# Kernel tuning notes

Hardware: AMD Instinct MI355X
Metric: run time of the kernel (lower is better)

The kernel has to match this reference:

```python
import jax, jax.numpy as jnp
from jax import lax
import numpy as np

B = 2; C = 128; H = 128; W = 128; NPIX = H * W
HTH = 184; HTW = 180; NBINS = HTH * HTW
NSPH = 16384; KHT = 8; KSPH = 16
N0, N1, N2 = 1024, 256, 64
K0, K1, K2 = 8, 8, 8
EPS = 1e-5


def setup_inputs() -> dict:
    key = jax.random.key(0)
    ks = jax.random.split(key, 24)
    f32 = jnp.float32
    inp = {}
    inp["image"] = jax.random.normal(ks[0], (B, C, H, W), f32)
    inp["bn_gamma"] = jnp.ones((C,), f32)
    inp["bn_beta"] = jnp.zeros((C,), f32)
    inp["ht_idx"] = jax.random.randint(ks[1], (NBINS, KHT), 0, NPIX, jnp.int32)
    inp["ht_w"] = jax.random.uniform(ks[2], (NBINS, KHT), f32)
    inp["w_htconv"] = jax.random.normal(ks[3], (3, 3, C, C), f32) / np.sqrt(9.0 * C)
    inp["htbn_gamma"] = jnp.ones((C,), f32)
    inp["htbn_beta"] = jnp.zeros((C,), f32)
    inp["sph_idx"] = jax.random.randint(ks[4], (NSPH, KSPH), 0, NBINS, jnp.int32)
    inp["sph_w"] = jax.random.uniform(ks[5], (NSPH, KSPH), f32)
    inp["w_sc"] = jax.random.normal(ks[6], (3, 64, C), f32) / np.sqrt(1.0 * C)
    inp["b_sc"] = jnp.zeros((3, 64), f32)
    inp["scbn_gamma"] = jnp.ones((3, 64), f32)
    inp["scbn_beta"] = jnp.zeros((3, 64), f32)
    inp["dgcn_w"] = jax.random.normal(ks[7], (3, 4, 128, 64), f32) / np.sqrt(128.0)
    inp["dgcn_b"] = jnp.zeros((3, 4, 64), f32)
    inp["dgcn_hw"] = jax.random.normal(ks[8], (3, 64), f32) / 8.0
    inp["dgcn_hb"] = jnp.zeros((3,), f32)
    inp["ind0"] = jax.random.randint(ks[9], (B, N0), 0, NSPH, jnp.int32)
    inp["ind1"] = jax.random.randint(ks[10], (B, 3, N1), 0, NSPH, jnp.int32)
    inp["ind2"] = jax.random.randint(ks[11], (B, 3, N2), 0, NSPH, jnp.int32)
    # kNN-style edges: structured centers (each node repeated k times), random neighbors
    c0 = jnp.tile(jnp.repeat(jnp.arange(N0, dtype=jnp.int32), K0)[None], (B, 1))
    inp["edge0"] = jnp.stack([c0, jax.random.randint(ks[12], (B, N0 * K0), 0, N0, jnp.int32)], 1)
    c1 = jnp.broadcast_to(jnp.repeat(jnp.arange(N1, dtype=jnp.int32), K1)[None, None], (B, 3, N1 * K1))
    inp["edge1"] = jnp.stack([c1, jax.random.randint(ks[13], (B, 3, N1 * K1), 0, N1, jnp.int32)], 2)
    c2 = jnp.broadcast_to(jnp.repeat(jnp.arange(N2, dtype=jnp.int32), K2)[None, None], (B, 3, N2 * K2))
    inp["edge2"] = jnp.stack([c2, jax.random.randint(ks[14], (B, 3, N2 * K2), 0, N2, jnp.int32)], 2)
    inp["target0"] = jax.random.randint(ks[15], (B, N0), 0, 2, jnp.int32)
    inp["target1"] = jax.random.randint(ks[16], (B * 3, N1), 0, 2, jnp.int32)
    inp["target2"] = jax.random.randint(ks[17], (B * 3, N2), 0, 2, jnp.int32)
    return inp


def _bn2d(x, g, b):
    m = x.mean((0, 2, 3), keepdims=True)
    v = x.var((0, 2, 3), keepdims=True)
    return g[None, :, None, None] * (x - m) * lax.rsqrt(v + EPS) + b[None, :, None, None]


def _sphere(x_htf, sph_idx, sph_w, ind):
    # x_htf: [B,C,NBINS]; ind: [B,S] -> weighted gather of HT bins per sphere node
    mi = sph_idx[ind]          # [B,S,K]
    mw = sph_w[ind]            # [B,S,K]
    g = jax.vmap(lambda xb, ib: xb[:, ib])(x_htf, mi)   # [B,C,S,K]
    return (g * mw[:, None]).sum(-1)                    # [B,C,S]


def _sconv(x, w, b, g, be):
    # 1x1 conv [B,C,S]->[B,64,S] + BN1d (batch stats) + ReLU
    y = jnp.einsum('oc,bcs->bos', w, x) + b[None, :, None]
    m = y.mean((0, 2), keepdims=True)
    v = y.var((0, 2), keepdims=True)
    return jax.nn.relu(g[None, :, None] * (y - m) * lax.rsqrt(v + EPS) + be[None, :, None])


def _dgcn(x, edge, ws, bs, hw, hb, n, k):
    # x: [Bg,n,64]; edge: [Bg,2,n*k] (row0=center, row1=neighbor); 4 EdgeConv layers
    for i in range(4):
        xc = jnp.take_along_axis(x, edge[:, 0, :, None], axis=1)   # [Bg,n*k,Cin]
        xn = jnp.take_along_axis(x, edge[:, 1, :, None], axis=1)
        h = jax.nn.relu(jnp.concatenate([xc, xn - xc], -1) @ ws[i] + bs[i])
        x = h.reshape(x.shape[0], n, k, -1).max(2)                 # max over neighbors
    return x @ hw + hb                                             # [Bg,n] logits


def _bce(logits, target):
    t = target.astype(logits.dtype)
    l = jnp.maximum(logits, 0.0) - logits * t + jnp.log1p(jnp.exp(-jnp.abs(logits)))
    pos = t > 0.5
    npos = jnp.maximum(pos.sum(), 1).astype(l.dtype)
    nneg = jnp.maximum((~pos).sum(), 1).astype(l.dtype)
    return jnp.where(pos, l, 0.0).sum() / npos, jnp.where(pos, 0.0, l).sum() / nneg


def _forward(image, bn_gamma, bn_beta, ht_idx, ht_w, w_htconv, htbn_gamma, htbn_beta,
             sph_idx, sph_w, w_sc, b_sc, scbn_gamma, scbn_beta,
             dgcn_w, dgcn_b, dgcn_hw, dgcn_hb,
             ind0, ind1, ind2, edge0, edge1, edge2, target0, target1, target2):
    x = jax.nn.relu(_bn2d(image, bn_gamma, bn_beta))
    xf = x.reshape(B, C, NPIX)
    # Hough voting: each HT bin accumulates KHT weighted pixels
    ht = (xf[:, :, ht_idx] * ht_w).sum(-1).reshape(B, C, HTH, HTW)
    hc = lax.conv_general_dilated(ht, w_htconv, (1, 1), 'SAME',
                                  dimension_numbers=('NCHW', 'HWIO', 'NCHW'))
    x_htf = jax.nn.relu(_bn2d(hc, htbn_gamma, htbn_beta)).reshape(B, C, NBINS)

    # scale 0
    x0 = _sconv(_sphere(x_htf, sph_idx, sph_w, ind0),
                w_sc[0], b_sc[0], scbn_gamma[0], scbn_beta[0]).transpose(0, 2, 1)
    x0 = _dgcn(x0, edge0, dgcn_w[0], dgcn_b[0], dgcn_hw[0], dgcn_hb[0], N0, K0)   # [B,N0]
    # scale 1 (3 vanishing-point branches folded into batch)
    x1 = _sconv(_sphere(x_htf, sph_idx, sph_w, ind1.reshape(B, -1)),
                w_sc[1], b_sc[1], scbn_gamma[1], scbn_beta[1]).transpose(0, 2, 1)
    x1 = _dgcn(x1.reshape(B * 3, N1, 64), edge1.reshape(B * 3, 2, N1 * K1),
               dgcn_w[1], dgcn_b[1], dgcn_hw[1], dgcn_hb[1], N1, K1)              # [B*3,N1]
    # scale 2
    x2 = _sconv(_sphere(x_htf, sph_idx, sph_w, ind2.reshape(B, -1)),
                w_sc[2], b_sc[2], scbn_gamma[2], scbn_beta[2]).transpose(0, 2, 1)
    x2 = _dgcn(x2.reshape(B * 3, N2, 64), edge2.reshape(B * 3, 2, N2 * K2),
               dgcn_w[2], dgcn_b[2], dgcn_hw[2], dgcn_hb[2], N2, K2)              # [B*3,N2]

    lp0, ln0 = _bce(x0, target0)
    lp1, ln1 = _bce(x1, target1)
    lp2, ln2 = _bce(x2, target2)
    losses = jnp.stack([lp0, ln0, lp1, ln1, lp2, ln2])
    preds = jnp.concatenate([jax.nn.sigmoid(x0).reshape(B, -1),
                             jax.nn.sigmoid(x1).reshape(B, -1),
                             jax.nn.sigmoid(x2).reshape(B, -1)], axis=1)
    return losses, preds


def reference(image, bn_gamma, bn_beta, ht_idx, ht_w, w_htconv, htbn_gamma, htbn_beta,
              sph_idx, sph_w, w_sc, b_sc, scbn_gamma, scbn_beta,
              dgcn_w, dgcn_b, dgcn_hw, dgcn_hb,
              ind0, ind1, ind2, edge0, edge1, edge2, target0, target1, target2):
    return _forward(image, bn_gamma, bn_beta, ht_idx, ht_w, w_htconv, htbn_gamma, htbn_beta,
                    sph_idx, sph_w, w_sc, b_sc, scbn_gamma, scbn_beta,
                    dgcn_w, dgcn_b, dgcn_hw, dgcn_hb,
                    ind0, ind1, ind2, edge0, edge1, edge2, target0, target1, target2)
```

## Files before the change

kernel.cpp:

```cpp
#include <hip/hip_runtime.h>
#include <math.h>

#define B_ 2
#define C_ 128
#define NPIX_ 16384
#define HTH_ 184
#define HTW_ 180
#define NBINS_ 33120
#define PH_ 186
#define PW_ 184
#define NPB_ 1984
#define TOTN_ 3968
#define EPS_ 1e-5f

#define ST_HC_SUM 0
#define ST_HC_SQ  128
#define ST_SC_SUM 256
#define ST_SC_SQ  448
#define ST_LOSS   640
#define ST_IMG_S1 1472
#define ST_IMG_S2 1600

typedef __attribute__((ext_vector_type(8))) short v8s;
typedef __attribute__((ext_vector_type(4))) float v4f;

__device__ inline unsigned short f2b(float f) {
  unsigned u = __builtin_bit_cast(unsigned, f);
  unsigned r = u + 0x7fffu + ((u >> 16) & 1u);
  return (unsigned short)(r >> 16);
}
__device__ inline float b2f(unsigned short u) {
  unsigned v = ((unsigned)u) << 16;
  return __builtin_bit_cast(float, v);
}

__global__ void kprep(const float* __restrict__ w, const float* __restrict__ dw,
                      unsigned short* __restrict__ wtb, unsigned short* __restrict__ dwb,
                      unsigned* __restrict__ htb2) {
  int idx = blockIdx.x*256 + threadIdx.x;
  if (idx < 147456) {
    int tap = idx >> 14, z = idx & 16383;
    int j = z & 7, lane = (z >> 3) & 63, nt = (z >> 9) & 7, kt = (z >> 12) & 3;
    int l = lane & 15, q = lane >> 4;
    int co = nt*16 + l, ci = kt*32 + q*8 + j;
    wtb[idx] = f2b(w[(tap*C_ + ci)*C_ + co]);
  } else if (idx < 245760) {
    int i2 = idx - 147456;
    int sl = i2 >> 13, z = i2 & 8191;
    int j = z & 7, lane = (z >> 3) & 63, nt = (z >> 9) & 3, kt = (z >> 11) & 3;
    int l = lane & 15, q = lane >> 4;
    int co = nt*16 + l, cc = kt*32 + q*8 + j;
    dwb[i2] = f2b(dw[(sl*128 + cc)*64 + co]);
  } else {
    int i = idx - 245760;
    int d = i & 63;
    int cell = i >> 6;
    int b = cell / 1112, j = cell % 1112;
    int y, x;
    if (j < 184) { y = 0; x = j; }
    else if (j < 368) { y = 185; x = j - 184; }
    else { int c = j - 368; int xi = c / 186; y = c % 186; x = xi == 0 ? 0 : 180 + xi; }
    htb2[((size_t)(b*PH_ + y)*PW_ + x)*64 + d] = 0u;
  }
}

__global__ void k1_img_stats(const float* __restrict__ img, float* __restrict__ st) {
  int c = blockIdx.x; int chunk = blockIdx.y; int tid = threadIdx.x;
  float s1 = 0.f, s2 = 0.f;
  for (int i = chunk*4096 + tid; i < (chunk+1)*4096; i += 256) {
    int b = i >> 14, p = i & (NPIX_-1);
    float v = img[((size_t)(b*C_ + c))*NPIX_ + p];
    s1 += v; s2 += v*v;
  }
  __shared__ float r1[256], r2[256];
  r1[tid] = s1; r2[tid] = s2; __syncthreads();
  for (int off = 128; off; off >>= 1) {
    if (tid < off) { r1[tid] += r1[tid+off]; r2[tid] += r2[tid+off]; }
    __syncthreads();
  }
  if (tid == 0) {
    atomicAdd(&st[ST_IMG_S1 + c], r1[0]);
    atomicAdd(&st[ST_IMG_S2 + c], r2[0]);
  }
}

__global__ void k2_bnrelu_t(const float* __restrict__ img, const float* __restrict__ st,
                            const float* __restrict__ g, const float* __restrict__ be,
                            unsigned short* __restrict__ xt) {
  __shared__ float tile[32*65];
  __shared__ float ash[32], dsh[32];
  int p0 = blockIdx.x*64, c0 = blockIdx.y*32, b = blockIdx.z;
  int tid = threadIdx.x;
  if (tid < 32) {
    int c = c0 + tid;
    float n = (float)(B_*NPIX_);
    float m = st[ST_IMG_S1+c]/n;
    float var = st[ST_IMG_S2+c]/n - m*m;
    float a = g[c]*rsqrtf(var + EPS_);
    ash[tid] = a; dsh[tid] = be[c] - a*m;
  }
  __syncthreads();
  for (int r = 0; r < 8; r++) {
    int flat = tid + r*256;
    int row = flat >> 6, col = flat & 63;
    float v = img[((size_t)(b*C_ + c0 + row))*NPIX_ + p0 + col];
    tile[row*65 + col] = fmaxf(ash[row]*v + dsh[row], 0.f);
  }
  __syncthreads();
  for (int r = 0; r < 4; r++) {
    int flat = (tid + r*256)*2;
    int pl = flat >> 5, cl = flat & 31;
    unsigned lo = f2b(tile[cl*65 + pl]);
    unsigned hi = f2b(tile[(cl+1)*65 + pl]);
    *(unsigned*)&xt[((size_t)b*NPIX_ + p0 + pl)*C_ + c0 + cl] = lo | (hi << 16);
  }
}

__global__ void k3_hough(const unsigned* __restrict__ xt2, const int* __restrict__ hidx,
                         const float* __restrict__ hwt, unsigned* __restrict__ htb2) {
  int tid = threadIdx.x;
  int wv = __builtin_amdgcn_readfirstlane(tid >> 6);
  int bin = blockIdx.x*4 + wv;
  int b = blockIdx.y;
  int lane = tid & 63;
  const unsigned* base = xt2 + (size_t)b*NPIX_*64 + lane;
  float acc0 = 0.f, acc1 = 0.f;
  #pragma unroll
  for (int k = 0; k < 8; k++) {
    int p = hidx[bin*8 + k];
    float w = hwt[bin*8 + k];
    unsigned dv = base[(size_t)p*64];
    acc0 += w * b2f((unsigned short)(dv & 0xffff));
    acc1 += w * b2f((unsigned short)(dv >> 16));
  }
  int y = bin / HTW_, x = bin - y*HTW_;
  unsigned lo = f2b(acc0), hi = f2b(acc1);
  htb2[((size_t)(b*PH_ + y + 1)*PW_ + (x+1))*64 + lane] = lo | (hi << 16);
}

__global__ __launch_bounds__(256, 4) void k4_mfma(
    const unsigned short* __restrict__ htb, const unsigned short* __restrict__ wtb,
    unsigned short* __restrict__ hcb, float* __restrict__ st) {
  __shared__ char smem[33792];
  int tid = threadIdx.x;
  int w = tid >> 6, lane = tid & 63;
  int quad = lane >> 4, l16 = lane & 15;
  int ph = w & 1, ch = w >> 1;
  int b = blockIdx.z;
  int x0 = blockIdx.x*64;
  int y0 = blockIdx.y*2;
  const v8s* wbase = (const v8s*)wtb + lane;
  v4f acc[4][4];
  #pragma unroll
  for (int t = 0; t < 4; t++)
    #pragma unroll
    for (int nt = 0; nt < 4; nt++) acc[t][nt] = (v4f){0,0,0,0};

  for (int half = 0; half < 2; half++) {
    __syncthreads();
    #pragma unroll
    for (int it = 0; it < 9; it++) {
      int c = tid + it*256;
      if (c < 2112) {
        int px = c >> 3, part = c & 7;
        int r = px/66, xc = px - r*66;
        int gx = x0 + xc; if (gx > PW_-1) gx = PW_-1;
        const uint4* gp = (const uint4*)(htb + (((size_t)(b*PH_ + y0 + r))*PW_ + gx)*C_ + half*64) + part;
        *(uint4*)(smem + px*128 + ((part ^ (xc & 7)) << 4)) = *gp;
      }
    }
    __syncthreads();
    #pragma unroll
    for (int dy = 0; dy < 3; dy++) {
      #pragma unroll
      for (int dx = 0; dx < 3; dx++) {
        int sw = ((l16 + dx) & 7) << 4;
        int rowbase = ((ph + dy)*66 + l16 + dx)*128;
        #pragma unroll
        for (int kt2 = 0; kt2 < 2; kt2++) {
          int qo = quad*16 + kt2*64;
          v8s a[4];
          #pragma unroll
          for (int t = 0; t < 4; t++)
            a[t] = *(const v8s*)(smem + rowbase + t*2048 + (qo ^ sw));
          int kt = half*2 + kt2;
          #pragma unroll
          for (int nt = 0; nt < 4; nt++) {
            v8s bf = wbase[(((dy*3 + dx)*4 + kt)*8 + ch*4 + nt)*64];
            #pragma unroll
            for (int t = 0; t < 4; t++)
              acc[t][nt] = __builtin_amdgcn_mfma_f32_16x16x32_bf16(a[t], bf, acc[t][nt], 0, 0, 0);
          }
        }
      }
    }
  }
  __syncthreads();
  float* red = (float*)smem;
  int y = y0 + ph;
  float s1[4] = {0,0,0,0}, s2[4] = {0,0,0,0};
  #pragma unroll
  for (int t = 0; t < 4; t++) {
    #pragma unroll
    for (int nt = 0; nt < 4; nt++) {
      int co = ch*64 + nt*16 + l16;
      #pragma unroll
      for (int reg = 0; reg < 4; reg++) {
        int x = x0 + t*16 + quad*4 + reg;
        if (x < HTW_) {
          float v = acc[t][nt][reg];
          hcb[((size_t)b*NBINS_ + y*HTW_ + x)*C_ + co] = f2b(v);
          s1[nt] += v; s2[nt] += v*v;
        }
      }
    }
  }
  int slot = ph*4 + quad;
  #pragma unroll
  for (int nt = 0; nt < 4; nt++) red[(ch*64 + nt*16 + l16)*9 + slot] = s1[nt];
  __syncthreads();
  if (tid < 128) {
    float s = 0.f;
    #pragma unroll
    for (int k = 0; k < 8; k++) s += red[tid*9 + k];
    atomicAdd(&st[ST_HC_SUM + tid], s);
  }
  __syncthreads();
  #pragma unroll
  for (int nt = 0; nt < 4; nt++) red[(ch*64 + nt*16 + l16)*9 + slot] = s2[nt];
  __syncthreads();
  if (tid < 128) {
    float s = 0.f;
    #pragma unroll
    for (int k = 0; k < 8; k++) s += red[tid*9 + k];
    atomicAdd(&st[ST_HC_SQ + tid], s);
  }
}

__global__ void k6_sphere(const unsigned* __restrict__ hcb2, const float* __restrict__ st,
                          const float* __restrict__ g, const float* __restrict__ be,
                          const int* __restrict__ sph_idx, const float* __restrict__ sph_w,
                          const int* __restrict__ ind0, const int* __restrict__ ind1,
                          const int* __restrict__ ind2, float* __restrict__ out) {
  int tid = threadIdx.x;
  int wv = __builtin_amdgcn_readfirstlane(tid >> 6);
  int gn = blockIdx.x*4 + wv;
  int lane = tid & 63;
  int b = gn / NPB_, nb = gn % NPB_;
  int v;
  if (nb < 1024) v = ind0[b*1024 + nb];
  else if (nb < 1792) v = ind1[b*768 + nb - 1024];
  else v = ind2[b*192 + nb - 1792];
  int c0 = lane*2, c1 = c0 + 1;
  float n = (float)(B_*NBINS_);
  float m0 = st[ST_HC_SUM + c0]/n, m1 = st[ST_HC_SUM + c1]/n;
  float va0 = st[ST_HC_SQ + c0]/n - m0*m0, va1 = st[ST_HC_SQ + c1]/n - m1*m1;
  float a0 = g[c0]*rsqrtf(va0 + EPS_), a1 = g[c1]*rsqrtf(va1 + EPS_);
  float d0 = be[c0] - a0*m0, d1 = be[c1] - a1*m1;
  const unsigned* base = hcb2 + (size_t)b*NBINS_*64 + lane;
  float acc0 = 0.f, acc1 = 0.f;
  #pragma unroll
  for (int k = 0; k < 16; k++) {
    int mi = sph_idx[v*16 + k];
    float mw = sph_w[v*16 + k];
    unsigned dv = base[(size_t)mi*64];
    acc0 += mw * fmaxf(a0*b2f((unsigned short)(dv & 0xffff)) + d0, 0.f);
    acc1 += mw * fmaxf(a1*b2f((unsigned short)(dv >> 16)) + d1, 0.f);
  }
  *(float2*)&out[(size_t)gn*C_ + c0] = make_float2(acc0, acc1);
}

__global__ __launch_bounds__(256) void k7_sconv(
    const float* __restrict__ xin, const float* __restrict__ w_sc,
    const float* __restrict__ b_sc, float* __restrict__ y, float* __restrict__ st) {
  __shared__ float xs[32*128];
  __shared__ float wT[128*65];
  __shared__ float red[256];
  int tid = threadIdx.x;
  int gn0 = blockIdx.x * 32;
  int nb = gn0 % NPB_;
  int s = nb < 1024 ? 0 : (nb < 1792 ? 1 : 2);
  for (int r = 0; r < 16; r++) {
    int flat = tid + r*256;
    xs[flat] = xin[(size_t)gn0*C_ + flat];
  }
  for (int r = 0; r < 32; r++) {
    int flat = tid + r*256;
    int o = flat >> 7, cc = flat & 127;
    wT[cc*65 + o] = w_sc[(s*64 + o)*C_ + cc];
  }
  __syncthreads();
  int o = tid & 63, nl = tid >> 6;
  float bias = b_sc[s*64 + o];
  float acc[8];
  #pragma unroll
  for (int i = 0; i < 8; i++) acc[i] = bias;
  for (int cc = 0; cc < 128; cc++) {
    float wv = wT[cc*65 + o];
    #pragma unroll
    for (int i = 0; i < 8; i++)
      acc[i] += xs[(nl*8 + i)*128 + cc] * wv;
  }
  float s1 = 0.f, s2 = 0.f;
  #pragma unroll
  for (int i = 0; i < 8; i++) {
    y[(size_t)(gn0 + nl*8 + i)*64 + o] = acc[i];
    s1 += acc[i]; s2 += acc[i]*acc[i];
  }
  red[tid] = s1; __syncthreads();
  if (nl == 0) atomicAdd(&st[ST_SC_SUM + s*64 + o], red[o] + red[64+o] + red[128+o] + red[192+o]);
  __syncthreads();
  red[tid] = s2; __syncthreads();
  if (nl == 0) atomicAdd(&st[ST_SC_SQ + s*64 + o], red[o] + red[64+o] + red[128+o] + red[192+o]);
}

__global__ __launch_bounds__(256) void k10_dgcn(
    const void* __restrict__ xin_, unsigned short* __restrict__ xout,
    const int* __restrict__ edge0, const int* __restrict__ edge1, const int* __restrict__ edge2,
    const unsigned short* __restrict__ dwb, const float* __restrict__ db,
    const float* __restrict__ st, const float* __restrict__ scg, const float* __restrict__ scb,
    int layer, int usebn) {
  __shared__ unsigned short E[128*136];
  __shared__ float ash[64], dsh[64];
  int tid = threadIdx.x;
  int bid = blockIdx.x;
  int s, node_base, le_blk, span; const int* ec;
  if (bid < 128) {
    s = 0; int b = bid >> 6; node_base = b*NPB_; le_blk = (bid & 63)*128;
    span = 8192; ec = edge0 + b*2*8192;
  } else if (bid < 224) {
    int j = bid - 128; s = 1; int seg = j >> 4; int b = seg/3, vp = seg%3;
    node_base = b*NPB_ + 1024 + vp*256; le_blk = (j & 15)*128;
    span = 2048; ec = edge1 + ((b*3+vp)*2)*2048;
  } else {
    int j = bid - 224; s = 2; int seg = j >> 2; int b = seg/3, vp = seg%3;
    node_base = b*NPB_ + 1792 + vp*64; le_blk = (j & 3)*128;
    span = 512; ec = edge2 + ((b*3+vp)*2)*512;
  }
  const int* en = ec + span;
  if (usebn) {
    if (tid < 64) {
      float n = s==0 ? 2048.f : (s==1 ? 1536.f : 384.f);
      float m = st[ST_SC_SUM + s*64 + tid]/n;
      float var = st[ST_SC_SQ + s*64 + tid]/n - m*m;
      float a = scg[s*64 + tid]*rsqrtf(var + EPS_);
      ash[tid] = a; dsh[tid] = scb[s*64 + tid] - a*m;
    }
    __syncthreads();
  }
  {
    int r = tid >> 1, h = tid & 1;
    int e = le_blk + r;
    int ci = ec[e], ni = en[e];
    if (usebn) {
      const float* xc = (const float*)xin_ + (size_t)(node_base + ci)*64;
      const float* xn = (const float*)xin_ + (size_t)(node_base + ni)*64;
      #pragma unroll
      for (int c8 = 0; c8 < 64; c8 += 8) {
        v8s pk;
        #pragma unroll
        for (int j = 0; j < 8; j++) {
          int c = c8 + j;
          float vc = fmaxf(ash[c]*xc[c] + dsh[c], 0.f);
          float val = vc;
          if (h) val = fmaxf(ash[c]*xn[c] + dsh[c], 0.f) - vc;
          pk[j] = (short)f2b(val);
        }
        *(v8s*)&E[r*136 + h*64 + c8] = pk;
      }
    } else {
      const unsigned short* xc = (const unsigned short*)xin_ + (size_t)(node_base + ci)*64;
      const unsigned short* xn = (const unsigned short*)xin_ + (size_t)(node_base + ni)*64;
      #pragma unroll
      for (int c8 = 0; c8 < 64; c8 += 8) {
        v8s vc8 = *(const v8s*)&xc[c8];
        v8s pk = vc8;
        if (h) {
          v8s vn8 = *(const v8s*)&xn[c8];
          #pragma unroll
          for (int j = 0; j < 8; j++)
            pk[j] = (short)f2b(b2f((unsigned short)vn8[j]) - b2f((unsigned short)vc8[j]));
        }
        *(v8s*)&E[r*136 + h*64 + c8] = pk;
      }
    }
  }
  __syncthreads();
  int wave = tid >> 6, lane = tid & 63;
  int quad = lane >> 4, l16 = lane & 15;
  const unsigned short* wb = dwb + (size_t)(s*4 + layer)*8192;
  v4f acc[2][4];
  #pragma unroll
  for (int t = 0; t < 2; t++)
    #pragma unroll
    for (int nt = 0; nt < 4; nt++) acc[t][nt] = (v4f){0,0,0,0};
  #pragma unroll
  for (int kt = 0; kt < 4; kt++) {
    v8s a0 = *(const v8s*)&E[(wave*32 + l16)*136 + quad*8 + kt*32];
    v8s a1 = *(const v8s*)&E[(wave*32 + 16 + l16)*136 + quad*8 + kt*32];
    #pragma unroll
    for (int nt = 0; nt < 4; nt++) {
      v8s bf = *(const v8s*)&wb[((kt*4 + nt)*64 + lane)*8];
      acc[0][nt] = __builtin_amdgcn_mfma_f32_16x16x32_bf16(a0, bf, acc[0][nt], 0, 0, 0);
      acc[1][nt] = __builtin_amdgcn_mfma_f32_16x16x32_bf16(a1, bf, acc[1][nt], 0, 0, 0);
    }
  }
  int vb0 = le_blk/8 + wave*4;
  #pragma unroll
  for (int t = 0; t < 2; t++) {
    #pragma unroll
    for (int nt = 0; nt < 4; nt++) {
      float bias = db[(s*4 + layer)*64 + nt*16 + l16];
      float m = fmaxf(fmaxf(acc[t][nt][0], acc[t][nt][1]),
                      fmaxf(acc[t][nt][2], acc[t][nt][3]));
      m = fmaxf(m + bias, 0.f);
      float other = __shfl_xor(m, 16);
      m = fmaxf(m, other);
      if ((quad & 1) == 0) {
        int v = vb0 + t*2 + (quad >> 1);
        xout[(size_t)(node_base + v)*64 + nt*16 + l16] = f2b(m);
      }
    }
  }
}

__global__ __launch_bounds__(256) void k11_head(
    const unsigned short* __restrict__ x, const float* __restrict__ hw, const float* __restrict__ hb,
    const int* __restrict__ t0, const int* __restrict__ t1, const int* __restrict__ t2,
    float* __restrict__ out, float* __restrict__ st) {
  __shared__ float shw[192];
  int tid = threadIdx.x;
  if (tid < 192) shw[tid] = hw[tid];
  __syncthreads();
  int gn = blockIdx.x*256 + tid;
  bool valid = gn < TOTN_;
  int g = valid ? gn : TOTN_-1;
  int b = g / NPB_, nb = g % NPB_;
  int s, tg;
  if (nb < 1024) { s = 0; tg = t0[b*1024 + nb]; }
  else if (nb < 1792) { s = 1; int j = nb-1024; tg = t1[(b*3 + (j>>8))*256 + (j&255)]; }
  else { s = 2; int j = nb-1792; tg = t2[(b*3 + (j>>6))*64 + (j&63)]; }
  const unsigned short* row = x + (size_t)g*64;
  float logit = hb[s];
  #pragma unroll
  for (int c8 = 0; c8 < 64; c8 += 8) {
    v8s v = *(const v8s*)&row[c8];
    #pragma unroll
    for (int j = 0; j < 8; j++)
      logit += b2f((unsigned short)v[j]) * shw[s*64 + c8 + j];
  }
  if (valid) out[6 + gn] = 1.f / (1.f + expf(-logit));
  float tf = (float)tg;
  float l = fmaxf(logit, 0.f) - logit*tf + log1pf(expf(-fabsf(logit)));
  float sp = (valid && tg) ? l : 0.f;
  float sn = (valid && !tg) ? l : 0.f;
  float cp = (valid && tg) ? 1.f : 0.f;
  float cn = (valid && !tg) ? 1.f : 0.f;
  for (int off = 32; off; off >>= 1) {
    sp += __shfl_down(sp, off);
    sn += __shfl_down(sn, off);
    cp += __shfl_down(cp, off);
    cn += __shfl_down(cn, off);
  }
  if ((tid & 63) == 0) {
    atomicAdd(&st[ST_LOSS + s*4 + 0], sp);
    atomicAdd(&st[ST_LOSS + s*4 + 1], sn);
    atomicAdd(&st[ST_LOSS + s*4 + 2], cp);
    atomicAdd(&st[ST_LOSS + s*4 + 3], cn);
  }
}

__global__ void k12_fin(const float* __restrict__ st, float* __restrict__ out) {
  int i = threadIdx.x;
  if (i < 6) {
    int s = i >> 1; int pos = !(i & 1);
    float sum = st[ST_LOSS + s*4 + (pos ? 0 : 1)];
    float cnt = st[ST_LOSS + s*4 + (pos ? 2 : 3)];
    out[i] = sum / fmaxf(cnt, 1.f);
  }
}

extern "C" void kernel_launch(void* const* d_in, const int* in_sizes, int n_in,
                              void* d_out, int out_size, void* d_ws, size_t ws_size,
                              hipStream_t stream) {
  const float* image  = (const float*)d_in[0];
  const float* bn_g   = (const float*)d_in[1];
  const float* bn_b   = (const float*)d_in[2];
  const int*   ht_idx = (const int*)  d_in[3];
  const float* ht_w   = (const float*)d_in[4];
  const float* w_conv = (const float*)d_in[5];
  const float* htbn_g = (const float*)d_in[6];
  const float* htbn_b = (const float*)d_in[7];
  const int*   sph_idx= (const int*)  d_in[8];
  const float* sph_w  = (const float*)d_in[9];
  const float* w_sc   = (const float*)d_in[10];
  const float* b_sc   = (const float*)d_in[11];
  const float* scbn_g = (const float*)d_in[12];
  const float* scbn_b = (const float*)d_in[13];
  const float* dgcn_w = (const float*)d_in[14];
  const float* dgcn_b = (const float*)d_in[15];
  const float* dgcn_hw= (const float*)d_in[16];
  const float* dgcn_hb= (const float*)d_in[17];
  const int*   ind0   = (const int*)  d_in[18];
  const int*   ind1   = (const int*)  d_in[19];
  const int*   ind2   = (const int*)  d_in[20];
  const int*   edge0  = (const int*)  d_in[21];
  const int*   edge1  = (const int*)  d_in[22];
  const int*   edge2  = (const int*)  d_in[23];
  const int*   t0     = (const int*)  d_in[24];
  const int*   t1     = (const int*)  d_in[25];
  const int*   t2     = (const int*)  d_in[26];
  float* out = (float*)d_out;

  char* ws = (char*)d_ws;
  unsigned short* x_t   = (unsigned short*)(ws);
  unsigned short* htb   = (unsigned short*)(ws +  8388608);
  unsigned short* hcb   = (unsigned short*)(ws + 25911296);
  unsigned short* wtb   = (unsigned short*)(ws + 42868736);
  unsigned short* dwb   = (unsigned short*)(ws + 43163648);
  float*          sph_o = (float*)(ws + 43360256);
  float*          y_sc  = (float*)(ws + 45391872);
  unsigned short* xdgA  = (unsigned short*)(ws + 46407680);
  unsigned short* xdgB  = (unsigned short*)(ws + 46915584);
  float*          st    = (float*)(ws + 47423488);

  hipMemsetAsync(st, 0, 1728*sizeof(float), stream);
  kprep<<<1516, 256, 0, stream>>>(w_conv, dgcn_w, wtb, dwb, (unsigned*)htb);
  k1_img_stats<<<dim3(128,8), 256, 0, stream>>>(image, st);
  k2_bnrelu_t<<<dim3(256,4,2), 256, 0, stream>>>(image, st, bn_g, bn_b, x_t);
  k3_hough<<<dim3(NBINS_/4, B_), 256, 0, stream>>>((const unsigned*)x_t, ht_idx, ht_w, (unsigned*)htb);
  k4_mfma<<<dim3(3, 92, 2), 256, 0, stream>>>(htb, wtb, hcb, st);
  k6_sphere<<<TOTN_/4, 256, 0, stream>>>((const unsigned*)hcb, st, htbn_g, htbn_b, sph_idx, sph_w, ind0, ind1, ind2, sph_o);
  k7_sconv<<<TOTN_/32, 256, 0, stream>>>(sph_o, w_sc, b_sc, y_sc, st);
  k10_dgcn<<<248, 256, 0, stream>>>((const void*)y_sc, xdgA, edge0, edge1, edge2, dwb, dgcn_b, st, scbn_g, scbn_b, 0, 1);
  k10_dgcn<<<248, 256, 0, stream>>>((const void*)xdgA, xdgB, edge0, edge1, edge2, dwb, dgcn_b, st, scbn_g, scbn_b, 1, 0);
  k10_dgcn<<<248, 256, 0, stream>>>((const void*)xdgB, xdgA, edge0, edge1, edge2, dwb, dgcn_b, st, scbn_g, scbn_b, 2, 0);
  k10_dgcn<<<248, 256, 0, stream>>>((const void*)xdgA, xdgB, edge0, edge1, edge2, dwb, dgcn_b, st, scbn_g, scbn_b, 3, 0);
  k11_head<<<16, 256, 0, stream>>>(xdgB, dgcn_hw, dgcn_hb, t0, t1, t2, out, st);
  k12_fin<<<1, 64, 0, stream>>>(st, out);
}
```

Before: 267.8 us.

## Fuse prep with image stats, restructure conv MFMA, fuse sphere gather with sconv

Merges the weight/padding prep kernel with the image-statistics kernel into one launch. Rewrites the 3x3 Hough conv so each wave computes 32 flat output bins across all 128 output channels, loading activations straight from global memory and staging only each tap's weights in shared memory. Fuses the sphere gather with the sphere conv so gathered features stay in shared memory instead of round-tripping through a global buffer. This trades the earlier shared-memory halo reuse of activations for simpler indexing and fewer launches, and the fused sphere kernel now has far fewer blocks to spread the gather work over.

Result: faster. 249.3 us (-6.9%).

```diff
diff --git a/kernel.cpp b/kernel.cpp
--- a/kernel.cpp
+++ b/kernel.cpp
@@ -34,53 +34,57 @@
   return __builtin_bit_cast(float, v);
 }
 
-__global__ void kprep(const float* __restrict__ w, const float* __restrict__ dw,
-                      unsigned short* __restrict__ wtb, unsigned short* __restrict__ dwb,
-                      unsigned* __restrict__ htb2) {
-  int idx = blockIdx.x*256 + threadIdx.x;
-  if (idx < 147456) {
-    int tap = idx >> 14, z = idx & 16383;
-    int j = z & 7, lane = (z >> 3) & 63, nt = (z >> 9) & 7, kt = (z >> 12) & 3;
-    int l = lane & 15, q = lane >> 4;
-    int co = nt*16 + l, ci = kt*32 + q*8 + j;
-    wtb[idx] = f2b(w[(tap*C_ + ci)*C_ + co]);
-  } else if (idx < 245760) {
-    int i2 = idx - 147456;
-    int sl = i2 >> 13, z = i2 & 8191;
-    int j = z & 7, lane = (z >> 3) & 63, nt = (z >> 9) & 3, kt = (z >> 11) & 3;
-    int l = lane & 15, q = lane >> 4;
-    int co = nt*16 + l, cc = kt*32 + q*8 + j;
-    dwb[i2] = f2b(dw[(sl*128 + cc)*64 + co]);
+__global__ void kprep0(const float* __restrict__ w, const float* __restrict__ dw,
+                       unsigned short* __restrict__ wtb, unsigned short* __restrict__ dwb,
+                       unsigned* __restrict__ htb2, const float* __restrict__ img,
+                       float* __restrict__ st) {
+  int bid = blockIdx.x;
+  int tid = threadIdx.x;
+  if (bid < 1516) {
+    int idx = bid*256 + tid;
+    if (idx < 147456) {
+      int tap = idx >> 14, z = idx & 16383;
+      int j = z & 7, lane = (z >> 3) & 63, nt = (z >> 9) & 7, kt = (z >> 12) & 3;
+      int l = lane & 15, q = lane >> 4;
+      int co = nt*16 + l, ci = kt*32 + q*8 + j;
+      wtb[idx] = f2b(w[(tap*C_ + ci)*C_ + co]);
+    } else if (idx < 245760) {
+      int i2 = idx - 147456;
+      int sl = i2 >> 13, z = i2 & 8191;
+      int j = z & 7, lane = (z >> 3) & 63, nt = (z >> 9) & 3, kt = (z >> 11) & 3;
+      int l = lane & 15, q = lane >> 4;
+      int co = nt*16 + l, cc = kt*32 + q*8 + j;
+      dwb[i2] = f2b(dw[(sl*128 + cc)*64 + co]);
+    } else if (idx < 388096) {
+      int i = idx - 245760;
+      int d = i & 63;
+      int cell = i >> 6;
+      int b = cell / 1112, j = cell % 1112;
+      int y, x;
+      if (j < 184) { y = 0; x = j; }
+      else if (j < 368) { y = 185; x = j - 184; }
+      else { int c = j - 368; int xi = c / 186; y = c % 186; x = xi == 0 ? 0 : 180 + xi; }
+      htb2[((size_t)(b*PH_ + y)*PW_ + x)*64 + d] = 0u;
+    }
   } else {
-    int i = idx - 245760;
-    int d = i & 63;
-    int cell = i >> 6;
-    int b = cell / 1112, j = cell % 1112;
-    int y, x;
-    if (j < 184) { y = 0; x = j; }
-    else if (j < 368) { y = 185; x = j - 184; }
-    else { int c = j - 368; int xi = c / 186; y = c % 186; x = xi == 0 ? 0 : 180 + xi; }
-    htb2[((size_t)(b*PH_ + y)*PW_ + x)*64 + d] = 0u;
-  }
-}
-
-__global__ void k1_img_stats(const float* __restrict__ img, float* __restrict__ st) {
-  int c = blockIdx.x; int chunk = blockIdx.y; int tid = threadIdx.x;
-  float s1 = 0.f, s2 = 0.f;
-  for (int i = chunk*4096 + tid; i < (chunk+1)*4096; i += 256) {
-    int b = i >> 14, p = i & (NPIX_-1);
-    float v = img[((size_t)(b*C_ + c))*NPIX_ + p];
-    s1 += v; s2 += v*v;
-  }
-  __shared__ float r1[256], r2[256];
-  r1[tid] = s1; r2[tid] = s2; __syncthreads();
-  for (int off = 128; off; off >>= 1) {
-    if (tid < off) { r1[tid] += r1[tid+off]; r2[tid] += r2[tid+off]; }
-    __syncthreads();
-  }
-  if (tid == 0) {
-    atomicAdd(&st[ST_IMG_S1 + c], r1[0]);
-    atomicAdd(&st[ST_IMG_S2 + c], r2[0]);
+    int kb = bid - 1516;
+    int c = kb >> 3, chunk = kb & 7;
+    float s1 = 0.f, s2 = 0.f;
+    for (int i = chunk*4096 + tid; i < (chunk+1)*4096; i += 256) {
+      int b = i >> 14, p = i & (NPIX_-1);
+      float v = img[((size_t)(b*C_ + c))*NPIX_ + p];
+      s1 += v; s2 += v*v;
+    }
+    __shared__ float r1[256], r2[256];
+    r1[tid] = s1; r2[tid] = s2; __syncthreads();
+    for (int off = 128; off; off >>= 1) {
+      if (tid < off) { r1[tid] += r1[tid+off]; r2[tid] += r2[tid+off]; }
+      __syncthreads();
+    }
+    if (tid == 0) {
+      atomicAdd(&st[ST_IMG_S1 + c], r1[0]);
+      atomicAdd(&st[ST_IMG_S2 + c], r2[0]);
+    }
   }
 }
 
@@ -138,151 +142,139 @@
   htb2[((size_t)(b*PH_ + y + 1)*PW_ + (x+1))*64 + lane] = lo | (hi << 16);
 }
 
-__global__ __launch_bounds__(256, 4) void k4_mfma(
+__global__ __launch_bounds__(256, 3) void k4_mfma(
     const unsigned short* __restrict__ htb, const unsigned short* __restrict__ wtb,
     unsigned short* __restrict__ hcb, float* __restrict__ st) {
-  __shared__ char smem[33792];
-  int tid = threadIdx.x;
-  int w = tid >> 6, lane = tid & 63;
+  __shared__ char smem[32768];
+  int tid = threadIdx.x;
+  int wav = tid >> 6, lane = tid & 63;
   int quad = lane >> 4, l16 = lane & 15;
-  int ph = w & 1, ch = w >> 1;
-  int b = blockIdx.z;
-  int x0 = blockIdx.x*64;
-  int y0 = blockIdx.y*2;
-  const v8s* wbase = (const v8s*)wtb + lane;
-  v4f acc[4][4];
-  #pragma unroll
-  for (int t = 0; t < 4; t++)
-    #pragma unroll
-    for (int nt = 0; nt < 4; nt++) acc[t][nt] = (v4f){0,0,0,0};
-
-  for (int half = 0; half < 2; half++) {
+  int b = blockIdx.y;
+  int p0 = blockIdx.x*128 + wav*32;
+  size_t ab[2];
+  #pragma unroll
+  for (int t = 0; t < 2; t++) {
+    int px = p0 + t*16 + l16; if (px > NBINS_-1) px = NBINS_-1;
+    int y = px / HTW_, x = px % HTW_;
+    ab[t] = (((size_t)(b*PH_ + y))*PW_ + x)*C_ + quad*8;
+  }
+  v4f acc[2][8];
+  #pragma unroll
+  for (int t = 0; t < 2; t++)
+    #pragma unroll
+    for (int nt = 0; nt < 8; nt++) acc[t][nt] = (v4f){0,0,0,0};
+
+  for (int tap = 0; tap < 9; tap++) {
     __syncthreads();
-    #pragma unroll
-    for (int it = 0; it < 9; it++) {
-      int c = tid + it*256;
-      if (c < 2112) {
-        int px = c >> 3, part = c & 7;
-        int r = px/66, xc = px - r*66;
-        int gx = x0 + xc; if (gx > PW_-1) gx = PW_-1;
-        const uint4* gp = (const uint4*)(htb + (((size_t)(b*PH_ + y0 + r))*PW_ + gx)*C_ + half*64) + part;
-        *(uint4*)(smem + px*128 + ((part ^ (xc & 7)) << 4)) = *gp;
+    const uint4* src = (const uint4*)(wtb + tap*16384);
+    uint4* dst = (uint4*)smem;
+    #pragma unroll
+    for (int s = 0; s < 8; s++) dst[tid + s*256] = src[tid + s*256];
+    __syncthreads();
+    int dy = tap/3, dx = tap - dy*3;
+    int toff = (dy*PW_ + dx)*C_;
+    v8s a[2][4];
+    #pragma unroll
+    for (int t = 0; t < 2; t++)
+      #pragma unroll
+      for (int kt = 0; kt < 4; kt++)
+        a[t][kt] = *(const v8s*)&htb[ab[t] + toff + kt*32];
+    #pragma unroll
+    for (int kt = 0; kt < 4; kt++) {
+      #pragma unroll
+      for (int nt = 0; nt < 8; nt++) {
+        v8s bf = *(const v8s*)(smem + ((((kt*8 + nt)*64) + lane) << 4));
+        acc[0][nt] = __builtin_amdgcn_mfma_f32_16x16x32_bf16(a[0][kt], bf, acc[0][nt], 0, 0, 0);
+        acc[1][nt] = __builtin_amdgcn_mfma_f32_16x16x32_bf16(a[1][kt], bf, acc[1][nt], 0, 0, 0);
       }
     }
-    __syncthreads();
-    #pragma unroll
-    for (int dy = 0; dy < 3; dy++) {
-      #pragma unroll
-      for (int dx = 0; dx < 3; dx++) {
-        int sw = ((l16 + dx) & 7) << 4;
-        int rowbase = ((ph + dy)*66 + l16 + dx)*128;
-        #pragma unroll
-        for (int kt2 = 0; kt2 < 2; kt2++) {
-          int qo = quad*16 + kt2*64;
-          v8s a[4];
-          #pragma unroll
-          for (int t = 0; t < 4; t++)
-            a[t] = *(const v8s*)(smem + rowbase + t*2048 + (qo ^ sw));
-          int kt = half*2 + kt2;
-          #pragma unroll
-          for (int nt = 0; nt < 4; nt++) {
-            v8s bf = wbase[(((dy*3 + dx)*4 + kt)*8 + ch*4 + nt)*64];
-            #pragma unroll
-            for (int t = 0; t < 4; t++)
-              acc[t][nt] = __builtin_amdgcn_mfma_f32_16x16x32_bf16(a[t], bf, acc[t][nt], 0, 0, 0);
-          }
-        }
-      }
-    }
   }
   __syncthreads();
   float* red = (float*)smem;
-  int y = y0 + ph;
-  float s1[4] = {0,0,0,0}, s2[4] = {0,0,0,0};
-  #pragma unroll
-  for (int t = 0; t < 4; t++) {
-    #pragma unroll
-    for (int nt = 0; nt < 4; nt++) {
-      int co = ch*64 + nt*16 + l16;
+  float s1[8], s2[8];
+  #pragma unroll
+  for (int nt = 0; nt < 8; nt++) { s1[nt] = 0.f; s2[nt] = 0.f; }
+  #pragma unroll
+  for (int t = 0; t < 2; t++) {
+    int pbase = p0 + t*16 + quad*4;
+    #pragma unroll
+    for (int nt = 0; nt < 8; nt++) {
+      int co = nt*16 + l16;
       #pragma unroll
       for (int reg = 0; reg < 4; reg++) {
-        int x = x0 + t*16 + quad*4 + reg;
-        if (x < HTW_) {
+        int po = pbase + reg;
+        if (po < NBINS_) {
           float v = acc[t][nt][reg];
-          hcb[((size_t)b*NBINS_ + y*HTW_ + x)*C_ + co] = f2b(v);
+          hcb[((size_t)b*NBINS_ + po)*C_ + co] = f2b(v);
           s1[nt] += v; s2[nt] += v*v;
         }
       }
     }
   }
-  int slot = ph*4 + quad;
-  #pragma unroll
-  for (int nt = 0; nt < 4; nt++) red[(ch*64 + nt*16 + l16)*9 + slot] = s1[nt];
+  int slot = wav*4 + quad;
+  #pragma unroll
+  for (int nt = 0; nt < 8; nt++) red[(nt*16 + l16)*17 + slot] = s1[nt];
   __syncthreads();
   if (tid < 128) {
     float s = 0.f;
     #pragma unroll
-    for (int k = 0; k < 8; k++) s += red[tid*9 + k];
+    for (int k = 0; k < 16; k++) s += red[tid*17 + k];
     atomicAdd(&st[ST_HC_SUM + tid], s);
   }
   __syncthreads();
   #pragma unroll
-  for (int nt = 0; nt < 4; nt++) red[(ch*64 + nt*16 + l16)*9 + slot] = s2[nt];
+  for (int nt = 0; nt < 8; nt++) red[(nt*16 + l16)*17 + slot] = s2[nt];
   __syncthreads();
   if (tid < 128) {
     float s = 0.f;
     #pragma unroll
-    for (int k = 0; k < 8; k++) s += red[tid*9 + k];
+    for (int k = 0; k < 16; k++) s += red[tid*17 + k];
     atomicAdd(&st[ST_HC_SQ + tid], s);
   }
 }
 
-__global__ void k6_sphere(const unsigned* __restrict__ hcb2, const float* __restrict__ st,
-                          const float* __restrict__ g, const float* __restrict__ be,
-                          const int* __restrict__ sph_idx, const float* __restrict__ sph_w,
-                          const int* __restrict__ ind0, const int* __restrict__ ind1,
-                          const int* __restrict__ ind2, float* __restrict__ out) {
-  int tid = threadIdx.x;
-  int wv = __builtin_amdgcn_readfirstlane(tid >> 6);
-  int gn = blockIdx.x*4 + wv;
-  int lane = tid & 63;
-  int b = gn / NPB_, nb = gn % NPB_;
-  int v;
-  if (nb < 1024) v = ind0[b*1024 + nb];
-  else if (nb < 1792) v = ind1[b*768 + nb - 1024];
-  else v = ind2[b*192 + nb - 1792];
-  int c0 = lane*2, c1 = c0 + 1;
-  float n = (float)(B_*NBINS_);
-  float m0 = st[ST_HC_SUM + c0]/n, m1 = st[ST_HC_SUM + c1]/n;
-  float va0 = st[ST_HC_SQ + c0]/n - m0*m0, va1 = st[ST_HC_SQ + c1]/n - m1*m1;
-  float a0 = g[c0]*rsqrtf(va0 + EPS_), a1 = g[c1]*rsqrtf(va1 + EPS_);
-  float d0 = be[c0] - a0*m0, d1 = be[c1] - a1*m1;
-  const unsigned* base = hcb2 + (size_t)b*NBINS_*64 + lane;
-  float acc0 = 0.f, acc1 = 0.f;
-  #pragma unroll
-  for (int k = 0; k < 16; k++) {
-    int mi = sph_idx[v*16 + k];
-    float mw = sph_w[v*16 + k];
-    unsigned dv = base[(size_t)mi*64];
-    acc0 += mw * fmaxf(a0*b2f((unsigned short)(dv & 0xffff)) + d0, 0.f);
-    acc1 += mw * fmaxf(a1*b2f((unsigned short)(dv >> 16)) + d1, 0.f);
-  }
-  *(float2*)&out[(size_t)gn*C_ + c0] = make_float2(acc0, acc1);
-}
-
-__global__ __launch_bounds__(256) void k7_sconv(
-    const float* __restrict__ xin, const float* __restrict__ w_sc,
-    const float* __restrict__ b_sc, float* __restrict__ y, float* __restrict__ st) {
+__global__ __launch_bounds__(256) void k67_sphconv(
+    const unsigned* __restrict__ hcb2, const float* __restrict__ g, const float* __restrict__ be,
+    const int* __restrict__ sph_idx, const float* __restrict__ sph_w,
+    const int* __restrict__ ind0, const int* __restrict__ ind1, const int* __restrict__ ind2,
+    const float* __restrict__ w_sc, const float* __restrict__ b_sc,
+    float* __restrict__ y, float* __restrict__ st) {
   __shared__ float xs[32*128];
   __shared__ float wT[128*65];
   __shared__ float red[256];
   int tid = threadIdx.x;
-  int gn0 = blockIdx.x * 32;
-  int nb = gn0 % NPB_;
-  int s = nb < 1024 ? 0 : (nb < 1792 ? 1 : 2);
-  for (int r = 0; r < 16; r++) {
-    int flat = tid + r*256;
-    xs[flat] = xin[(size_t)gn0*C_ + flat];
+  int gn0 = blockIdx.x*32;
+  int nb0 = gn0 % NPB_;
+  int s = nb0 < 1024 ? 0 : (nb0 < 1792 ? 1 : 2);
+  int wv = tid >> 6, lane = tid & 63;
+  {
+    int c0 = lane*2, c1 = c0 + 1;
+    float n = (float)(B_*NBINS_);
+    float m0 = st[ST_HC_SUM + c0]/n, m1 = st[ST_HC_SUM + c1]/n;
+    float va0 = st[ST_HC_SQ + c0]/n - m0*m0, va1 = st[ST_HC_SQ + c1]/n - m1*m1;
+    float a0 = g[c0]*rsqrtf(va0 + EPS_), a1 = g[c1]*rsqrtf(va1 + EPS_);
+    float d0 = be[c0] - a0*m0, d1 = be[c1] - a1*m1;
+    for (int i = 0; i < 8; i++) {
+      int node_l = wv*8 + i;
+      int gn = gn0 + node_l;
+      int b = gn / NPB_, nb = gn % NPB_;
+      int v;
+      if (nb < 1024) v = ind0[b*1024 + nb];
+      else if (nb < 1792) v = ind1[b*768 + nb - 1024];
+      else v = ind2[b*192 + nb - 1792];
+      v = __builtin_amdgcn_readfirstlane(v);
+      const unsigned* base = hcb2 + (size_t)b*NBINS_*64 + lane;
+      float acc0 = 0.f, acc1 = 0.f;
+      #pragma unroll
+      for (int k = 0; k < 16; k++) {
+        int mi = sph_idx[v*16 + k];
+        float mw = sph_w[v*16 + k];
+        unsigned dv = base[(size_t)mi*64];
+        acc0 += mw * fmaxf(a0*b2f((unsigned short)(dv & 0xffff)) + d0, 0.f);
+        acc1 += mw * fmaxf(a1*b2f((unsigned short)(dv >> 16)) + d1, 0.f);
+      }
+      *(float2*)&xs[node_l*128 + c0] = make_float2(acc0, acc1);
+    }
   }
   for (int r = 0; r < 32; r++) {
     int flat = tid + r*256;
@@ -296,10 +288,10 @@
   #pragma unroll
   for (int i = 0; i < 8; i++) acc[i] = bias;
   for (int cc = 0; cc < 128; cc++) {
-    float wv = wT[cc*65 + o];
+    float wvv = wT[cc*65 + o];
     #pragma unroll
     for (int i = 0; i < 8; i++)
-      acc[i] += xs[(nl*8 + i)*128 + cc] * wv;
+      acc[i] += xs[(nl*8 + i)*128 + cc] * wvv;
   }
   float s1 = 0.f, s2 = 0.f;
   #pragma unroll
@@ -518,20 +510,18 @@
   unsigned short* hcb   = (unsigned short*)(ws + 25911296);
   unsigned short* wtb   = (unsigned short*)(ws + 42868736);
   unsigned short* dwb   = (unsigned short*)(ws + 43163648);
-  float*          sph_o = (float*)(ws + 43360256);
-  float*          y_sc  = (float*)(ws + 45391872);
-  unsigned short* xdgA  = (unsigned short*)(ws + 46407680);
-  unsigned short* xdgB  = (unsigned short*)(ws + 46915584);
-  float*          st    = (float*)(ws + 47423488);
+  float*          y_sc  = (float*)(ws + 43360256);
+  unsigned short* xdgA  = (unsigned short*)(ws + 44376064);
+  unsigned short* xdgB  = (unsigned short*)(ws + 44883968);
+  float*          st    = (float*)(ws + 45391872);
 
   hipMemsetAsync(st, 0, 1728*sizeof(float), stream);
-  kprep<<<1516, 256, 0, stream>>>(w_conv, dgcn_w, wtb, dwb, (unsigned*)htb);
-  k1_img_stats<<<dim3(128,8), 256, 0, stream>>>(image, st);
+  kprep0<<<2540, 256, 0, stream>>>(w_conv, dgcn_w, wtb, dwb, (unsigned*)htb, image, st);
   k2_bnrelu_t<<<dim3(256,4,2), 256, 0, stream>>>(image, st, bn_g, bn_b, x_t);
   k3_hough<<<dim3(NBINS_/4, B_), 256, 0, stream>>>((const unsigned*)x_t, ht_idx, ht_w, (unsigned*)htb);
-  k4_mfma<<<dim3(3, 92, 2), 256, 0, stream>>>(htb, wtb, hcb, st);
-  k6_sphere<<<TOTN_/4, 256, 0, stream>>>((const unsigned*)hcb, st, htbn_g, htbn_b, sph_idx, sph_w, ind0, ind1, ind2, sph_o);
-  k7_sconv<<<TOTN_/32, 256, 0, stream>>>(sph_o, w_sc, b_sc, y_sc, st);
+  k4_mfma<<<dim3(259, 2), 256, 0, stream>>>(htb, wtb, hcb, st);
+  k67_sphconv<<<TOTN_/32, 256, 0, stream>>>((const unsigned*)hcb, htbn_g, htbn_b, sph_idx, sph_w,
+                                            ind0, ind1, ind2, w_sc, b_sc, y_sc, st);
   k10_dgcn<<<248, 256, 0, stream>>>((const void*)y_sc, xdgA, edge0, edge1, edge2, dwb, dgcn_b, st, scbn_g, scbn_b, 0, 1);
   k10_dgcn<<<248, 256, 0, stream>>>((const void*)xdgA, xdgB, edge0, edge1, edge2, dwb, dgcn_b, st, scbn_g, scbn_b, 1, 0);
   k10_dgcn<<<248, 256, 0, stream>>>((const void*)xdgB, xdgA, edge0, edge1, edge2, dwb, dgcn_b, st, scbn_g, scbn_b, 2, 0);
```
